# Performance work log

Hardware: AMD Instinct MI355X
Metric: run time of the kernel (lower is better)

## Reference

```python
import jax, jax.numpy as jnp
import numpy as np

NUM_PROTEINS = 19000
NUM_DRUGS = 4000
NUM_CELL_LINES = 16
BATCH = 4096
NUM_EDGES = 40000
LAYERS = [2048, 1024, 1]
IN_DIM = 2 * (NUM_PROTEINS + NUM_CELL_LINES)  # 38032


def setup_inputs() -> dict:
    key = jax.random.key(0)
    ks = jax.random.split(key, 10)
    inp = {
        "drug_pairs": jax.random.randint(ks[0], (BATCH, 2), 0, NUM_DRUGS, dtype=jnp.int64 if jax.config.jax_enable_x64 else jnp.int32),
        "cell_lines": jax.random.randint(ks[1], (BATCH,), 0, NUM_CELL_LINES),
        "dpi_drug": jax.random.randint(ks[2], (NUM_EDGES,), 0, NUM_DRUGS),
        "dpi_prot": jax.random.randint(ks[3], (NUM_EDGES,), 0, NUM_PROTEINS),
        "W0": jax.random.normal(ks[4], (LAYERS[0], IN_DIM), dtype=jnp.float32) * 0.02,
        "b0": jnp.zeros((LAYERS[0],), dtype=jnp.float32),
        "W1": jax.random.normal(ks[5], (LAYERS[1], LAYERS[0]), dtype=jnp.float32) * 0.02,
        "b1": jnp.zeros((LAYERS[1],), dtype=jnp.float32),
        "W2": jax.random.normal(ks[6], (LAYERS[2], LAYERS[1]), dtype=jnp.float32) * 0.02,
        "b2": jnp.zeros((LAYERS[2],), dtype=jnp.float32),
    }
    return inp


def _mlp(x, W0, b0, W1, b1, W2, b2):
    h = jax.nn.relu(x @ W0.T + b0)
    h = jax.nn.relu(h @ W1.T + b1)
    return h @ W2.T + b2


def reference(drug_pairs, cell_lines, dpi_drug, dpi_prot, W0, b0, W1, b1, W2, b2):
    # Build drug -> protein multi-hot table with a single vectorized scatter
    # (replaces the per-row Python loop: prot[i, targets] = 1)
    table = jnp.zeros((NUM_DRUGS, NUM_PROTEINS), dtype=jnp.float32)
    table = table.at[dpi_drug, dpi_prot].set(1.0)

    prot_1 = table[drug_pairs[:, 0]]  # [B, P]
    prot_2 = table[drug_pairs[:, 1]]  # [B, P]
    one_hot_cl = jax.nn.one_hot(cell_lines, NUM_CELL_LINES, dtype=jnp.float32)  # [B, C]

    bd1 = jnp.concatenate([prot_1, one_hot_cl], axis=1)
    bd2 = jnp.concatenate([prot_2, one_hot_cl], axis=1)
    x1 = jnp.concatenate([bd1, bd2], axis=1)  # [B, 2*(P+C)]
    x2 = jnp.concatenate([bd2, bd1], axis=1)

    out1 = _mlp(x1, W0, b0, W1, b1, W2, b2)
    out2 = _mlp(x2, W0, b0, W1, b1, W2, b2)
    return (out1[:, 0], out2[:, 0])
```

## Files before the change

### kernel.cpp

```cpp
#include <hip/hip_runtime.h>
#include <hip/hip_bf16.h>
#include <stdint.h>

#define NPROT 19000
#define NDRUG 4000
#define NCELL 16
#define BATCH 4096
#define NEDGE 40000
#define L0 2048
#define L1DIM 1024
#define INDIM 38032
#define HALFDIM 19016
#define DCAP 96
#define BMWORDS ((NDRUG * NPROT + 31) / 32)
#define PSPLIT 9504
#define WSLOT 9504
#define WSTN2 9512

typedef float f32x4 __attribute__((ext_vector_type(4)));
typedef short s16x8 __attribute__((ext_vector_type(8)));

__global__ void zero_all_kernel(int* __restrict__ p, int n) {
    int i = blockIdx.x * 256 + threadIdx.x;
    if (i < n) p[i] = 0;
}

__global__ void scatter_dedup_kernel(const int* __restrict__ drug, const int* __restrict__ prot,
                                     unsigned* __restrict__ bitmap, int* __restrict__ cnt2,
                                     int* __restrict__ cntTot, unsigned short* __restrict__ dlist) {
    int e = blockIdx.x * 256 + threadIdx.x;
    if (e < NEDGE) {
        int d = drug[e], p = prot[e];
        unsigned idx = (unsigned)d * NPROT + p;
        unsigned bit = 1u << (idx & 31u);
        unsigned old = atomicOr(&bitmap[idx >> 5], bit);
        if (!(old & bit)) {
            int ph = p >= PSPLIT;
            atomicAdd(&cnt2[d * 2 + ph], 1);
            int pos = atomicAdd(&cntTot[d], 1);
            if (pos < DCAP) dlist[d * DCAP + pos] = (unsigned short)p;
        }
    }
}

__global__ __launch_bounds__(512) void stream_meta_kernel(const int* __restrict__ cnt2,
                                                          int* __restrict__ wlen,
                                                          int* __restrict__ wbase,
                                                          int* __restrict__ pref,
                                                          int* __restrict__ tcnt) {
    __shared__ int wl[16];
    int t = threadIdx.x;
    if (t < 16) wl[t] = 0;
    __syncthreads();
    int c0 = 0, c1 = 0;
#pragma unroll
    for (int k = 0; k < 8; ++k) {
        int d = t + (k << 9);
        pref[((t << 3) + k) * 2 + 0] = c0;
        pref[((t << 3) + k) * 2 + 1] = c1;
        if (d < NDRUG) {
            int n0 = cnt2[d * 2], n1 = cnt2[d * 2 + 1];
            c0 += n0 ? n0 : 1;
            c1 += n1 ? n1 : 1;
        }
    }
    tcnt[t * 2] = c0;
    tcnt[t * 2 + 1] = c1;
    atomicMax(&wl[(t >> 6) * 2], c0);
    atomicMax(&wl[(t >> 6) * 2 + 1], c1);
    __syncthreads();
    if (t == 0) {
        int run = 0;
        for (int s = 0; s < 16; ++s) {
            wlen[s] = wl[s];
            wbase[s] = run;
            run += wl[s] * 64;
        }
    }
}

__global__ __launch_bounds__(256) void fill_stream_kernel(const int* __restrict__ cnt2,
                                                          const unsigned short* __restrict__ dlist,
                                                          const int* __restrict__ wbase,
                                                          const int* __restrict__ wlen,
                                                          const int* __restrict__ pref,
                                                          const int* __restrict__ tcnt,
                                                          unsigned short* __restrict__ estream) {
    int g = blockIdx.x * 256 + threadIdx.x;
    if (g < NDRUG) {
        int d = g;
        int t = d & 511, k = d >> 9;
        int wv = t >> 6, lane = t & 63;
        int n0 = cnt2[d * 2], n1 = cnt2[d * 2 + 1];
        int base0 = wbase[wv * 2 + 0] + lane;
        int base1 = wbase[wv * 2 + 1] + lane;
        int i0 = pref[((t << 3) + k) * 2 + 0];
        int i1 = pref[((t << 3) + k) * 2 + 1];
        int n = min(n0 + n1, DCAP);
        int j0 = 0, j1 = 0;
        for (int i = 0; i < n; ++i) {
            int p = dlist[d * DCAP + i];
            if (p < PSPLIT) {
                unsigned short e = (unsigned short)(p | ((j0 == n0 - 1) ? 0x8000 : 0));
                estream[base0 + (i0 + j0) * 64] = e;
                ++j0;
            } else {
                unsigned short e = (unsigned short)((p - PSPLIT) | ((j1 == n1 - 1) ? 0x8000 : 0));
                estream[base1 + (i1 + j1) * 64] = e;
                ++j1;
            }
        }
        if (n0 == 0) estream[base0 + i0 * 64] = (unsigned short)(WSLOT | 0x8000);
        if (n1 == 0) estream[base1 + i1 * 64] = (unsigned short)(WSLOT | 0x8000);
    } else if (g < NDRUG + 1024) {
        int idx = g - NDRUG;
        int t = idx >> 1, ph = idx & 1;
        int wv = t >> 6;
        int base = wbase[wv * 2 + ph] + (t & 63);
        int wl = wlen[wv * 2 + ph];
        for (int j = tcnt[t * 2 + ph]; j < wl; ++j)
            estream[base + j * 64] = (unsigned short)WSLOT;
    }
}

__global__ void base_kernel(const float* __restrict__ W0, const float* __restrict__ b0,
                            float* __restrict__ BASE) {
    int i = blockIdx.x * 256 + threadIdx.x;
    if (i < NCELL * L0) {
        int c = i >> 11, ch = i & 2047;
        const float* wr = W0 + (size_t)ch * INDIM;
        BASE[(size_t)c * L0 + ch] = b0[ch] + wr[NPROT + c] + wr[HALFDIM + NPROT + c];
    }
}

__device__ inline unsigned bfpair(float a, float b) {
    unsigned ua = __float_as_uint(a), ub = __float_as_uint(b);
    ua += 0x7fffu + ((ua >> 16) & 1u);
    ub += 0x7fffu + ((ub >> 16) & 1u);
    return (ua >> 16) | (ub & 0xffff0000u);
}
__device__ inline float bflo(unsigned w) { return __uint_as_float(w << 16); }
__device__ inline float bfhi(unsigned w) { return __uint_as_float(w & 0xffff0000u); }

__global__ __launch_bounds__(512) void drug_sum_kernel(const float* __restrict__ W0,
                                                       const unsigned short* __restrict__ estream,
                                                       const int* __restrict__ wbase,
                                                       const int* __restrict__ wlen,
                                                       uint2* __restrict__ SAT) {
    __shared__ uint2 wst[WSTN2];
    int t = threadIdx.x;
    int bid = blockIdx.x;
    int ph = bid >> 10;
    int k3 = bid & 1023;
    int hb = k3 >> 9;
    int quad = k3 & 511;
    int ch0 = quad * 4;
    size_t colbase = (size_t)hb * HALFDIM + (size_t)ph * PSPLIT;
    int pc = ph ? (NPROT - PSPLIT) : PSPLIT;

    int wv = t >> 6;
    int sid = wv * 2 + ph;
    int base = wbase[sid] + (t & 63);
    int wl = wlen[sid];
    int nfull = wl >> 3, rem = wl & 7;
    unsigned e[8];
    if (nfull > 0) {
#pragma unroll
        for (int k = 0; k < 8; ++k) e[k] = estream[base + k * 64];
        base += 512;
    }

    const float* sA = W0 + (size_t)(ch0 + 0) * INDIM + colbase;
    const float* sB = W0 + (size_t)(ch0 + 1) * INDIM + colbase;
    const float* sC = W0 + (size_t)(ch0 + 2) * INDIM + colbase;
    const float* sD = W0 + (size_t)(ch0 + 3) * INDIM + colbase;
#pragma unroll
    for (int k = 0; k < 4; ++k) {
        int i = t * 4 + k * 2048;
        float4 a = *(const float4*)(sA + i);
        float4 b = *(const float4*)(sB + i);
        float4 c = *(const float4*)(sC + i);
        float4 d = *(const float4*)(sD + i);
        uint4 q0, q1;
        q0.x = bfpair(a.x, b.x); q0.y = bfpair(c.x, d.x);
        q0.z = bfpair(a.y, b.y); q0.w = bfpair(c.y, d.y);
        q1.x = bfpair(a.z, b.z); q1.y = bfpair(c.z, d.z);
        q1.z = bfpair(a.w, b.w); q1.w = bfpair(c.w, d.w);
        *(uint4*)&wst[i] = q0;
        *(uint4*)&wst[i + 2] = q1;
    }
    {
        int i = t * 4 + 8192;
        if (i < pc) {
            float4 a = *(const float4*)(sA + i);
            float4 b = *(const float4*)(sB + i);
            float4 c = *(const float4*)(sC + i);
            float4 d = *(const float4*)(sD + i);
            uint4 q0, q1;
            q0.x = bfpair(a.x, b.x); q0.y = bfpair(c.x, d.x);
            q0.z = bfpair(a.y, b.y); q0.w = bfpair(c.y, d.y);
            q1.x = bfpair(a.z, b.z); q1.y = bfpair(c.z, d.z);
            q1.z = bfpair(a.w, b.w); q1.w = bfpair(c.w, d.w);
            *(uint4*)&wst[i] = q0;
            *(uint4*)&wst[i + 2] = q1;
        }
    }
    if (t < 8) { wst[WSLOT + t].x = 0u; wst[WSLOT + t].y = 0u; }
    __syncthreads();

    float x0 = 0.f, x1 = 0.f, x2 = 0.f, x3 = 0.f;
    int kk = 0;
    uint2* dstT = SAT + (size_t)bid * 4096;

    auto procBatch = [&](const unsigned* ev) {
        uint2 w[8];
#pragma unroll
        for (int k = 0; k < 8; ++k) w[k] = wst[ev[k] & 0x7fffu];
#pragma unroll
        for (int k = 0; k < 8; ++k) {
            x0 += bflo(w[k].x);
            x1 += bfhi(w[k].x);
            x2 += bflo(w[k].y);
            x3 += bfhi(w[k].y);
            if (ev[k] & 0x8000u) {
                uint2 v;
                v.x = bfpair(x0, x1);
                v.y = bfpair(x2, x3);
                dstT[t + (kk << 9)] = v;
                ++kk; x0 = 0.f; x1 = 0.f; x2 = 0.f; x3 = 0.f;
            }
        }
    };

    if (nfull > 0) {
        for (int it = 1; it < nfull; ++it) {
            unsigned f[8];
#pragma unroll
            for (int k = 0; k < 8; ++k) f[k] = estream[base + k * 64];
            base += 512;
            procBatch(e);
#pragma unroll
            for (int k = 0; k < 8; ++k) e[k] = f[k];
        }
        procBatch(e);
    }
    for (int k = 0; k < rem; ++k) {
        unsigned ev = estream[base + k * 64];
        uint2 w = wst[ev & 0x7fffu];
        x0 += bflo(w.x);
        x1 += bfhi(w.x);
        x2 += bflo(w.y);
        x3 += bfhi(w.y);
        if (ev & 0x8000u) {
            uint2 v;
            v.x = bfpair(x0, x1);
            v.y = bfpair(x2, x3);
            dstT[t + (kk << 9)] = v;
            ++kk; x0 = 0.f; x1 = 0.f; x2 = 0.f; x3 = 0.f;
        }
    }
}

__global__ __launch_bounds__(256) void combine_kernel(const uint2* __restrict__ SAT,
                                                      __hip_bfloat16* __restrict__ SAb,
                                                      __hip_bfloat16* __restrict__ SBb) {
    __shared__ float tile[4][32][33];
    int b = blockIdx.x;
    int hb = b / 2000;
    int rem = b % 2000;
    int q0 = (rem / 125) * 32;
    int d0 = (rem % 125) * 32;
    const uint2* inA = SAT + (size_t)(hb * 512) * 4096;
    const uint2* inB = SAT + (size_t)(1024 + hb * 512) * 4096;
    int tx = threadIdx.x & 31, ty = threadIdx.x >> 5;
#pragma unroll
    for (int r = 0; r < 32; r += 8) {
        int q = q0 + r + ty;
        uint2 a = inA[(size_t)q * 4096 + d0 + tx];
        uint2 c = inB[(size_t)q * 4096 + d0 + tx];
        tile[0][r + ty][tx] = bflo(a.x) + bflo(c.x);
        tile[1][r + ty][tx] = bfhi(a.x) + bfhi(c.x);
        tile[2][r + ty][tx] = bflo(a.y) + bflo(c.y);
        tile[3][r + ty][tx] = bfhi(a.y) + bfhi(c.y);
    }
    __syncthreads();
    __hip_bfloat16* out = hb ? SBb : SAb;
#pragma unroll
    for (int r = 0; r < 32; r += 8) {
        int d = d0 + r + ty;
        float x = tile[0][tx][r + ty];
        float y = tile[1][tx][r + ty];
        float z = tile[2][tx][r + ty];
        float w = tile[3][tx][r + ty];
        uint2 v;
        v.x = bfpair(x, y);
        v.y = bfpair(z, w);
        *(uint2*)(out + (size_t)d * L0 + (q0 + tx) * 4) = v;
    }
}

__global__ void cvtw1_kernel(const float* __restrict__ W1, __hip_bfloat16* __restrict__ W1b) {
    int i = blockIdx.x * 256 + threadIdx.x;
    const int n = L1DIM * L0 / 4;
    if (i < n) {
        float4 v = ((const float4*)W1)[i];
        uint2 q;
        q.x = bfpair(v.x, v.y);
        q.y = bfpair(v.z, v.w);
        ((uint2*)W1b)[i] = q;
    }
}

__global__ __launch_bounds__(256) void build_h_kernel(const int* __restrict__ dp,
                                                      const int* __restrict__ cl,
                                                      const __hip_bfloat16* __restrict__ SAb,
                                                      const __hip_bfloat16* __restrict__ SBb,
                                                      const float* __restrict__ BASE,
                                                      __hip_bfloat16* __restrict__ h1) {
    int b = blockIdx.x;
    int d1 = dp[2 * b], d2 = dp[2 * b + 1], c = cl[b];
    int ch = threadIdx.x * 8;
    const float* bs = BASE + (size_t)c * L0 + ch;
    uint4 ua1 = *(const uint4*)(SAb + (size_t)d1 * L0 + ch);
    uint4 ua2 = *(const uint4*)(SAb + (size_t)d2 * L0 + ch);
    uint4 us1 = *(const uint4*)(SBb + (size_t)d1 * L0 + ch);
    uint4 us2 = *(const uint4*)(SBb + (size_t)d2 * L0 + ch);
    float4 vb0 = *(const float4*)(bs);
    float4 vb1 = *(const float4*)(bs + 4);
    float bsv[8] = {vb0.x, vb0.y, vb0.z, vb0.w, vb1.x, vb1.y, vb1.z, vb1.w};
    unsigned a1w[4] = {ua1.x, ua1.y, ua1.z, ua1.w};
    unsigned a2w[4] = {ua2.x, ua2.y, ua2.z, ua2.w};
    unsigned s1w[4] = {us1.x, us1.y, us1.z, us1.w};
    unsigned s2w[4] = {us2.x, us2.y, us2.z, us2.w};
    float z1[8], z2[8];
#pragma unroll
    for (int k = 0; k < 4; ++k) {
        z1[2 * k]     = fmaxf(bsv[2 * k]     + bflo(a1w[k]) + bflo(s2w[k]), 0.f);
        z1[2 * k + 1] = fmaxf(bsv[2 * k + 1] + bfhi(a1w[k]) + bfhi(s2w[k]), 0.f);
        z2[2 * k]     = fmaxf(bsv[2 * k]     + bflo(a2w[k]) + bflo(s1w[k]), 0.f);
        z2[2 * k + 1] = fmaxf(bsv[2 * k + 1] + bfhi(a2w[k]) + bfhi(s1w[k]), 0.f);
    }
    uint4 o1, o2;
    o1.x = bfpair(z1[0], z1[1]); o1.y = bfpair(z1[2], z1[3]);
    o1.z = bfpair(z1[4], z1[5]); o1.w = bfpair(z1[6], z1[7]);
    o2.x = bfpair(z2[0], z2[1]); o2.y = bfpair(z2[2], z2[3]);
    o2.z = bfpair(z2[4], z2[5]); o2.w = bfpair(z2[6], z2[7]);
    *(uint4*)((__hip_bfloat16*)h1 + (size_t)b * L0 + ch) = o1;
    *(uint4*)((__hip_bfloat16*)h1 + (size_t)(BATCH + b) * L0 + ch) = o2;
}

__global__ void init_out_kernel(float* __restrict__ out, const float* __restrict__ b2, int n) {
    int i = blockIdx.x * 256 + threadIdx.x;
    if (i < n) out[i] = b2[0];
}

#define BM 128
#define BN 128
#define BK2 64
__global__ __launch_bounds__(256) void gemm_kernel(const __hip_bfloat16* __restrict__ A,
                                                   const __hip_bfloat16* __restrict__ B,
                                                   const float* __restrict__ bias,
                                                   const float* __restrict__ W2,
                                                   float* __restrict__ out,
                                                   int M, int N, int K) {
    __shared__ __hip_bfloat16 As[BM * BK2];
    __shared__ __hip_bfloat16 Bs[BN * BK2];
    int t = threadIdx.x;
    int bid = blockIdx.x;
    int xcd = bid & 7, ii2 = bid >> 3;
    int by = xcd * 8 + (ii2 >> 3);
    int bx = ii2 & 7;
    int brow = by * BM, bcol = bx * BN;
    int w = t >> 6, l = t & 63;
    int wr = w >> 1, wc = w & 1;
    f32x4 acc[4][4] = {};
    int row = l & 15, ko = (l >> 4) * 8;
    int swz = (row & 7) * 8;
    for (int k0 = 0; k0 < K; k0 += BK2) {
#pragma unroll
        for (int i = 0; i < 4; ++i) {
            int idx = i * 256 + t;
            int r = idx >> 3;
            int cb = ((idx & 7) ^ (r & 7)) * 8;
            __builtin_amdgcn_global_load_lds(
                (const __attribute__((address_space(1))) void*)(A + (size_t)(brow + r) * K + k0 + cb),
                (__attribute__((address_space(3))) void*)(&As[idx * 8]), 16, 0, 0);
            __builtin_amdgcn_global_load_lds(
                (const __attribute__((address_space(1))) void*)(B + (size_t)(bcol + r) * K + k0 + cb),
                (__attribute__((address_space(3))) void*)(&Bs[idx * 8]), 16, 0, 0);
        }
        __syncthreads();
#pragma unroll
        for (int ks = 0; ks < 2; ++ks) {
            int col = (ks * 32 + ko) ^ swz;
            s16x8 af[4], bfr[4];
#pragma unroll
            for (int m = 0; m < 4; ++m)
                af[m] = *(const s16x8*)(&As[(wr * 64 + m * 16 + row) * BK2 + col]);
#pragma unroll
            for (int n = 0; n < 4; ++n)
                bfr[n] = *(const s16x8*)(&Bs[(wc * 64 + n * 16 + row) * BK2 + col]);
#pragma unroll
            for (int m = 0; m < 4; ++m)
#pragma unroll
                for (int n = 0; n < 4; ++n)
                    acc[m][n] = __builtin_amdgcn_mfma_f32_16x16x32_bf16(af[m], bfr[n], acc[m][n], 0, 0, 0);
        }
        __syncthreads();
    }
    int cr = (l >> 4) * 4;
    int cc = l & 15;
#pragma unroll
    for (int m = 0; m < 4; ++m) {
        float s[4] = {0.f, 0.f, 0.f, 0.f};
#pragma unroll
        for (int n = 0; n < 4; ++n) {
            int gcol = bcol + wc * 64 + n * 16 + cc;
            float bv = bias[gcol];
            float wv = W2[gcol];
#pragma unroll
            for (int j = 0; j < 4; ++j) {
                float v = fmaxf(acc[m][n][j] + bv, 0.f);
                s[j] += v * wv;
            }
        }
#pragma unroll
        for (int mask = 1; mask < 16; mask <<= 1) {
#pragma unroll
            for (int j = 0; j < 4; ++j) s[j] += __shfl_xor(s[j], mask);
        }
        if (cc == 0) {
            int grow = brow + wr * 64 + m * 16 + cr;
#pragma unroll
            for (int j = 0; j < 4; ++j) atomicAdd(&out[grow + j], s[j]);
        }
    }
}

extern "C" void kernel_launch(void* const* d_in, const int* in_sizes, int n_in,
                              void* d_out, int out_size, void* d_ws, size_t ws_size,
                              hipStream_t stream) {
    const int* drug_pairs = (const int*)d_in[0];
    const int* cell_lines = (const int*)d_in[1];
    const int* dpi_drug = (const int*)d_in[2];
    const int* dpi_prot = (const int*)d_in[3];
    const float* W0 = (const float*)d_in[4];
    const float* b0 = (const float*)d_in[5];
    const float* W1 = (const float*)d_in[6];
    const float* b1 = (const float*)d_in[7];
    const float* W2 = (const float*)d_in[8];
    const float* b2 = (const float*)d_in[9];
    float* out = (float*)d_out;

    char* ws = (char*)d_ws;
    size_t off = 0;
    auto alloc = [&](size_t bytes) {
        char* p = ws + off;
        off += (bytes + 255) & ~(size_t)255;
        return p;
    };
    __hip_bfloat16* SAb = (__hip_bfloat16*)alloc((size_t)NDRUG * L0 * 2);
    __hip_bfloat16* SBb = (__hip_bfloat16*)alloc((size_t)NDRUG * L0 * 2);
    uint2* SAT = (uint2*)alloc((size_t)2048 * 4096 * 8);
    float* BASE = (float*)alloc((size_t)NCELL * L0 * 4);
    __hip_bfloat16* W1b = (__hip_bfloat16*)alloc((size_t)L1DIM * L0 * 2);
    __hip_bfloat16* h1 = (__hip_bfloat16*)alloc((size_t)2 * BATCH * L0 * 2);
    const int ZREG_N = BMWORDS + 3 * NDRUG;
    int* zreg = (int*)alloc((size_t)ZREG_N * 4);
    unsigned* bitmap = (unsigned*)zreg;
    int* cnt2 = zreg + BMWORDS;
    int* cntTot = zreg + BMWORDS + 2 * NDRUG;
    unsigned short* dlist = (unsigned short*)alloc((size_t)NDRUG * DCAP * 2);
    int* wlen = (int*)alloc(16 * 4);
    int* wbase = (int*)alloc(16 * 4);
    int* pref = (int*)alloc((size_t)512 * 8 * 2 * 4);
    int* tcnt = (int*)alloc((size_t)512 * 2 * 4);
    unsigned short* estream = (unsigned short*)alloc((size_t)64 * (NEDGE + 2 * NDRUG + 2048) * 2);

    zero_all_kernel<<<(ZREG_N + 255) / 256, 256, 0, stream>>>(zreg, ZREG_N);
    scatter_dedup_kernel<<<(NEDGE + 255) / 256, 256, 0, stream>>>(dpi_drug, dpi_prot,
                                                                  bitmap, cnt2, cntTot, dlist);
    stream_meta_kernel<<<1, 512, 0, stream>>>(cnt2, wlen, wbase, pref, tcnt);
    fill_stream_kernel<<<(NDRUG + 1024 + 255) / 256, 256, 0, stream>>>(cnt2, dlist, wbase,
                                                                       wlen, pref, tcnt, estream);
    base_kernel<<<(NCELL * L0 + 255) / 256, 256, 0, stream>>>(W0, b0, BASE);
    drug_sum_kernel<<<2048, 512, 0, stream>>>(W0, estream, wbase, wlen, SAT);
    combine_kernel<<<4000, 256, 0, stream>>>(SAT, SAb, SBb);
    cvtw1_kernel<<<(L1DIM * L0 / 4 + 255) / 256, 256, 0, stream>>>(W1, W1b);
    build_h_kernel<<<BATCH, 256, 0, stream>>>(drug_pairs, cell_lines, SAb, SBb, BASE, h1);
    init_out_kernel<<<(2 * BATCH + 255) / 256, 256, 0, stream>>>(out, b2, 2 * BATCH);
    gemm_kernel<<<(2 * BATCH / BM) * (L1DIM / BN), 256, 0, stream>>>(h1, W1b, b1, W2, out,
                                                                     2 * BATCH, L1DIM, L0);
}
```

Baseline: 216.7 us.

## Stage W0 channel pairs into LDS via direct global-to-LDS loads in fp32

The drug-sum kernel now handles two output channels per block instead of four. It copies the fp32 W0 rows straight into shared memory with global_load_lds, dropping the register round-trip and the bf16 packing during staging. Accumulation reads fp32 from LDS in two planes, and combine_kernel is adapted to the packed pair format. This doubles the block count and the SAT intermediate traffic in partial-sum launches, in exchange for cheaper staging and higher occupancy per block.

```diff
diff --git a/kernel.cpp b/kernel.cpp
--- a/kernel.cpp
+++ b/kernel.cpp
@@ -15,7 +15,7 @@
 #define BMWORDS ((NDRUG * NPROT + 31) / 32)
 #define PSPLIT 9504
 #define WSLOT 9504
-#define WSTN2 9512
+#define CPB 9512
 
 typedef float f32x4 __attribute__((ext_vector_type(4)));
 typedef short s16x8 __attribute__((ext_vector_type(8)));
@@ -146,17 +146,16 @@
                                                        const unsigned short* __restrict__ estream,
                                                        const int* __restrict__ wbase,
                                                        const int* __restrict__ wlen,
-                                                       uint2* __restrict__ SAT) {
-    __shared__ uint2 wst[WSTN2];
+                                                       unsigned* __restrict__ SAT) {
+    __shared__ float wst[2 * CPB];
     int t = threadIdx.x;
     int bid = blockIdx.x;
-    int ph = bid >> 10;
-    int k3 = bid & 1023;
-    int hb = k3 >> 9;
-    int quad = k3 & 511;
-    int ch0 = quad * 4;
+    int ph = bid >> 11;
+    int k3 = bid & 2047;
+    int hb = k3 >> 10;
+    int cp = k3 & 1023;
+    int ch0 = cp * 2;
     size_t colbase = (size_t)hb * HALFDIM + (size_t)ph * PSPLIT;
-    int pc = ph ? (NPROT - PSPLIT) : PSPLIT;
 
     int wv = t >> 6;
     int sid = wv * 2 + ph;
@@ -170,64 +169,38 @@
         base += 512;
     }
 
-    const float* sA = W0 + (size_t)(ch0 + 0) * INDIM + colbase;
-    const float* sB = W0 + (size_t)(ch0 + 1) * INDIM + colbase;
-    const float* sC = W0 + (size_t)(ch0 + 2) * INDIM + colbase;
-    const float* sD = W0 + (size_t)(ch0 + 3) * INDIM + colbase;
-#pragma unroll
-    for (int k = 0; k < 4; ++k) {
-        int i = t * 4 + k * 2048;
-        float4 a = *(const float4*)(sA + i);
-        float4 b = *(const float4*)(sB + i);
-        float4 c = *(const float4*)(sC + i);
-        float4 d = *(const float4*)(sD + i);
-        uint4 q0, q1;
-        q0.x = bfpair(a.x, b.x); q0.y = bfpair(c.x, d.x);
-        q0.z = bfpair(a.y, b.y); q0.w = bfpair(c.y, d.y);
-        q1.x = bfpair(a.z, b.z); q1.y = bfpair(c.z, d.z);
-        q1.z = bfpair(a.w, b.w); q1.w = bfpair(c.w, d.w);
-        *(uint4*)&wst[i] = q0;
-        *(uint4*)&wst[i + 2] = q1;
-    }
-    {
-        int i = t * 4 + 8192;
-        if (i < pc) {
-            float4 a = *(const float4*)(sA + i);
-            float4 b = *(const float4*)(sB + i);
-            float4 c = *(const float4*)(sC + i);
-            float4 d = *(const float4*)(sD + i);
-            uint4 q0, q1;
-            q0.x = bfpair(a.x, b.x); q0.y = bfpair(c.x, d.x);
-            q0.z = bfpair(a.y, b.y); q0.w = bfpair(c.y, d.y);
-            q1.x = bfpair(a.z, b.z); q1.y = bfpair(c.z, d.z);
-            q1.z = bfpair(a.w, b.w); q1.w = bfpair(c.w, d.w);
-            *(uint4*)&wst[i] = q0;
-            *(uint4*)&wst[i + 2] = q1;
-        }
-    }
-    if (t < 8) { wst[WSLOT + t].x = 0u; wst[WSLOT + t].y = 0u; }
+    const float* s0 = W0 + (size_t)ch0 * INDIM + colbase;
+    const float* s1 = W0 + (size_t)(ch0 + 1) * INDIM + colbase;
+    for (int i = t * 4; i < PSPLIT; i += 2048) {
+        __builtin_amdgcn_global_load_lds(
+            (const __attribute__((address_space(1))) void*)(s0 + i),
+            (__attribute__((address_space(3))) void*)(&wst[i]), 16, 0, 0);
+        __builtin_amdgcn_global_load_lds(
+            (const __attribute__((address_space(1))) void*)(s1 + i),
+            (__attribute__((address_space(3))) void*)(&wst[CPB + i]), 16, 0, 0);
+    }
+    if (t < 8) { wst[WSLOT + t] = 0.f; wst[CPB + WSLOT + t] = 0.f; }
     __syncthreads();
 
-    float x0 = 0.f, x1 = 0.f, x2 = 0.f, x3 = 0.f;
+    float x0 = 0.f, x1 = 0.f;
     int kk = 0;
-    uint2* dstT = SAT + (size_t)bid * 4096;
+    unsigned* dstT = SAT + (size_t)bid * 4096;
 
     auto procBatch = [&](const unsigned* ev) {
-        uint2 w[8];
-#pragma unroll
-        for (int k = 0; k < 8; ++k) w[k] = wst[ev[k] & 0x7fffu];
+        float w0[8], w1[8];
 #pragma unroll
         for (int k = 0; k < 8; ++k) {
-            x0 += bflo(w[k].x);
-            x1 += bfhi(w[k].x);
-            x2 += bflo(w[k].y);
-            x3 += bfhi(w[k].y);
+            int p = ev[k] & 0x7fffu;
+            w0[k] = wst[p];
+            w1[k] = wst[CPB + p];
+        }
+#pragma unroll
+        for (int k = 0; k < 8; ++k) {
+            x0 += w0[k];
+            x1 += w1[k];
             if (ev[k] & 0x8000u) {
-                uint2 v;
-                v.x = bfpair(x0, x1);
-                v.y = bfpair(x2, x3);
-                dstT[t + (kk << 9)] = v;
-                ++kk; x0 = 0.f; x1 = 0.f; x2 = 0.f; x3 = 0.f;
+                dstT[t + (kk << 9)] = bfpair(x0, x1);
+                ++kk; x0 = 0.f; x1 = 0.f;
             }
         }
     };
@@ -246,42 +219,33 @@
     }
     for (int k = 0; k < rem; ++k) {
         unsigned ev = estream[base + k * 64];
-        uint2 w = wst[ev & 0x7fffu];
-        x0 += bflo(w.x);
-        x1 += bfhi(w.x);
-        x2 += bflo(w.y);
-        x3 += bfhi(w.y);
+        int p = ev & 0x7fffu;
+        x0 += wst[p];
+        x1 += wst[CPB + p];
         if (ev & 0x8000u) {
-            uint2 v;
-            v.x = bfpair(x0, x1);
-            v.y = bfpair(x2, x3);
-            dstT[t + (kk << 9)] = v;
-            ++kk; x0 = 0.f; x1 = 0.f; x2 = 0.f; x3 = 0.f;
-        }
-    }
-}
-
-__global__ __launch_bounds__(256) void combine_kernel(const uint2* __restrict__ SAT,
+            dstT[t + (kk << 9)] = bfpair(x0, x1);
+            ++kk; x0 = 0.f; x1 = 0.f;
+        }
+    }
+}
+
+__global__ __launch_bounds__(256) void combine_kernel(const unsigned* __restrict__ SAT,
                                                       __hip_bfloat16* __restrict__ SAb,
                                                       __hip_bfloat16* __restrict__ SBb) {
-    __shared__ float tile[4][32][33];
+    __shared__ float tile[2][32][33];
     int b = blockIdx.x;
-    int hb = b / 2000;
-    int rem = b % 2000;
-    int q0 = (rem / 125) * 32;
+    int hb = b / 4000;
+    int rem = b % 4000;
+    int c0 = (rem / 125) * 32;
     int d0 = (rem % 125) * 32;
-    const uint2* inA = SAT + (size_t)(hb * 512) * 4096;
-    const uint2* inB = SAT + (size_t)(1024 + hb * 512) * 4096;
     int tx = threadIdx.x & 31, ty = threadIdx.x >> 5;
 #pragma unroll
     for (int r = 0; r < 32; r += 8) {
-        int q = q0 + r + ty;
-        uint2 a = inA[(size_t)q * 4096 + d0 + tx];
-        uint2 c = inB[(size_t)q * 4096 + d0 + tx];
-        tile[0][r + ty][tx] = bflo(a.x) + bflo(c.x);
-        tile[1][r + ty][tx] = bfhi(a.x) + bfhi(c.x);
-        tile[2][r + ty][tx] = bflo(a.y) + bflo(c.y);
-        tile[3][r + ty][tx] = bfhi(a.y) + bfhi(c.y);
+        int cp = c0 + r + ty;
+        unsigned a = SAT[(size_t)(hb * 1024 + cp) * 4096 + d0 + tx];
+        unsigned c = SAT[(size_t)(2048 + hb * 1024 + cp) * 4096 + d0 + tx];
+        tile[0][r + ty][tx] = bflo(a) + bflo(c);
+        tile[1][r + ty][tx] = bfhi(a) + bfhi(c);
     }
     __syncthreads();
     __hip_bfloat16* out = hb ? SBb : SAb;
@@ -290,12 +254,8 @@
         int d = d0 + r + ty;
         float x = tile[0][tx][r + ty];
         float y = tile[1][tx][r + ty];
-        float z = tile[2][tx][r + ty];
-        float w = tile[3][tx][r + ty];
-        uint2 v;
-        v.x = bfpair(x, y);
-        v.y = bfpair(z, w);
-        *(uint2*)(out + (size_t)d * L0 + (q0 + tx) * 4) = v;
+        unsigned v = bfpair(x, y);
+        *(unsigned*)(out + (size_t)d * L0 + (c0 + tx) * 2) = v;
     }
 }
 
@@ -461,7 +421,7 @@
     };
     __hip_bfloat16* SAb = (__hip_bfloat16*)alloc((size_t)NDRUG * L0 * 2);
     __hip_bfloat16* SBb = (__hip_bfloat16*)alloc((size_t)NDRUG * L0 * 2);
-    uint2* SAT = (uint2*)alloc((size_t)2048 * 4096 * 8);
+    unsigned* SAT = (unsigned*)alloc((size_t)4096 * 4096 * 4);
     float* BASE = (float*)alloc((size_t)NCELL * L0 * 4);
     __hip_bfloat16* W1b = (__hip_bfloat16*)alloc((size_t)L1DIM * L0 * 2);
     __hip_bfloat16* h1 = (__hip_bfloat16*)alloc((size_t)2 * BATCH * L0 * 2);
@@ -484,8 +444,8 @@
     fill_stream_kernel<<<(NDRUG + 1024 + 255) / 256, 256, 0, stream>>>(cnt2, dlist, wbase,
                                                                        wlen, pref, tcnt, estream);
     base_kernel<<<(NCELL * L0 + 255) / 256, 256, 0, stream>>>(W0, b0, BASE);
-    drug_sum_kernel<<<2048, 512, 0, stream>>>(W0, estream, wbase, wlen, SAT);
-    combine_kernel<<<4000, 256, 0, stream>>>(SAT, SAb, SBb);
+    drug_sum_kernel<<<4096, 512, 0, stream>>>(W0, estream, wbase, wlen, SAT);
+    combine_kernel<<<8000, 256, 0, stream>>>(SAT, SAb, SBb);
     cvtw1_kernel<<<(L1DIM * L0 / 4 + 255) / 256, 256, 0, stream>>>(W1, W1b);
     build_h_kernel<<<BATCH, 256, 0, stream>>>(drug_pairs, cell_lines, SAb, SBb, BASE, h1);
     init_out_kernel<<<(2 * BATCH + 255) / 256, 256, 0, stream>>>(out, b2, 2 * BATCH);
```

After: 222.8 us. 2.8% more time.

## Split protein range into four quarters with fp32 LDS staged via direct global-to-LDS loads

Applied to the files above, without the earlier changes.

Splits the protein dimension into four quarters instead of two, so each drug_sum block stages a smaller slice of W0. The slice stays in fp32 in LDS, one plane per output channel, loaded with global_load_lds instead of being converted to packed bf16 through registers. The smaller LDS footprint should allow more blocks per CU and removes the conversion work. In exchange the grid doubles, the SAT intermediate doubles in size, and combine_kernel must read and reduce four partial sums per element instead of two.

```diff
diff --git a/kernel.cpp b/kernel.cpp
--- a/kernel.cpp
+++ b/kernel.cpp
@@ -13,9 +13,9 @@
 #define HALFDIM 19016
 #define DCAP 96
 #define BMWORDS ((NDRUG * NPROT + 31) / 32)
-#define PSPLIT 9504
-#define WSLOT 9504
-#define WSTN2 9512
+#define PQ 4752
+#define QSLOT 4752
+#define QSTRIDE 4760
 
 typedef float f32x4 __attribute__((ext_vector_type(4)));
 typedef short s16x8 __attribute__((ext_vector_type(8)));
@@ -26,7 +26,7 @@
 }
 
 __global__ void scatter_dedup_kernel(const int* __restrict__ drug, const int* __restrict__ prot,
-                                     unsigned* __restrict__ bitmap, int* __restrict__ cnt2,
+                                     unsigned* __restrict__ bitmap, int* __restrict__ cnt4,
                                      int* __restrict__ cntTot, unsigned short* __restrict__ dlist) {
     int e = blockIdx.x * 256 + threadIdx.x;
     if (e < NEDGE) {
@@ -35,43 +35,53 @@
         unsigned bit = 1u << (idx & 31u);
         unsigned old = atomicOr(&bitmap[idx >> 5], bit);
         if (!(old & bit)) {
-            int ph = p >= PSPLIT;
-            atomicAdd(&cnt2[d * 2 + ph], 1);
+            int q = p / PQ;
+            atomicAdd(&cnt4[d * 4 + q], 1);
             int pos = atomicAdd(&cntTot[d], 1);
             if (pos < DCAP) dlist[d * DCAP + pos] = (unsigned short)p;
         }
     }
 }
 
-__global__ __launch_bounds__(512) void stream_meta_kernel(const int* __restrict__ cnt2,
+__global__ __launch_bounds__(512) void stream_meta_kernel(const int* __restrict__ cnt4,
                                                           int* __restrict__ wlen,
                                                           int* __restrict__ wbase,
                                                           int* __restrict__ pref,
                                                           int* __restrict__ tcnt) {
-    __shared__ int wl[16];
+    __shared__ int wl[32];
     int t = threadIdx.x;
-    if (t < 16) wl[t] = 0;
+    if (t < 32) wl[t] = 0;
     __syncthreads();
-    int c0 = 0, c1 = 0;
+    int c0 = 0, c1 = 0, c2 = 0, c3 = 0;
 #pragma unroll
     for (int k = 0; k < 8; ++k) {
         int d = t + (k << 9);
-        pref[((t << 3) + k) * 2 + 0] = c0;
-        pref[((t << 3) + k) * 2 + 1] = c1;
+        int pb = ((t << 3) + k) * 4;
+        pref[pb + 0] = c0;
+        pref[pb + 1] = c1;
+        pref[pb + 2] = c2;
+        pref[pb + 3] = c3;
         if (d < NDRUG) {
-            int n0 = cnt2[d * 2], n1 = cnt2[d * 2 + 1];
+            int n0 = cnt4[d * 4 + 0], n1 = cnt4[d * 4 + 1];
+            int n2 = cnt4[d * 4 + 2], n3 = cnt4[d * 4 + 3];
             c0 += n0 ? n0 : 1;
             c1 += n1 ? n1 : 1;
-        }
-    }
-    tcnt[t * 2] = c0;
-    tcnt[t * 2 + 1] = c1;
-    atomicMax(&wl[(t >> 6) * 2], c0);
-    atomicMax(&wl[(t >> 6) * 2 + 1], c1);
+            c2 += n2 ? n2 : 1;
+            c3 += n3 ? n3 : 1;
+        }
+    }
+    tcnt[t * 4 + 0] = c0;
+    tcnt[t * 4 + 1] = c1;
+    tcnt[t * 4 + 2] = c2;
+    tcnt[t * 4 + 3] = c3;
+    atomicMax(&wl[(t >> 6) * 4 + 0], c0);
+    atomicMax(&wl[(t >> 6) * 4 + 1], c1);
+    atomicMax(&wl[(t >> 6) * 4 + 2], c2);
+    atomicMax(&wl[(t >> 6) * 4 + 3], c3);
     __syncthreads();
     if (t == 0) {
         int run = 0;
-        for (int s = 0; s < 16; ++s) {
+        for (int s = 0; s < 32; ++s) {
             wlen[s] = wl[s];
             wbase[s] = run;
             run += wl[s] * 64;
@@ -79,7 +89,7 @@
     }
 }
 
-__global__ __launch_bounds__(256) void fill_stream_kernel(const int* __restrict__ cnt2,
+__global__ __launch_bounds__(256) void fill_stream_kernel(const int* __restrict__ cnt4,
                                                           const unsigned short* __restrict__ dlist,
                                                           const int* __restrict__ wbase,
                                                           const int* __restrict__ wlen,
@@ -91,35 +101,34 @@
         int d = g;
         int t = d & 511, k = d >> 9;
         int wv = t >> 6, lane = t & 63;
-        int n0 = cnt2[d * 2], n1 = cnt2[d * 2 + 1];
-        int base0 = wbase[wv * 2 + 0] + lane;
-        int base1 = wbase[wv * 2 + 1] + lane;
-        int i0 = pref[((t << 3) + k) * 2 + 0];
-        int i1 = pref[((t << 3) + k) * 2 + 1];
-        int n = min(n0 + n1, DCAP);
-        int j0 = 0, j1 = 0;
-        for (int i = 0; i < n; ++i) {
+        int n[4], bases[4], idx[4], j[4];
+#pragma unroll
+        for (int q = 0; q < 4; ++q) {
+            n[q] = cnt4[d * 4 + q];
+            bases[q] = wbase[wv * 4 + q] + lane;
+            idx[q] = pref[((t << 3) + k) * 4 + q];
+            j[q] = 0;
+        }
+        int ntot = min(n[0] + n[1] + n[2] + n[3], DCAP);
+        for (int i = 0; i < ntot; ++i) {
             int p = dlist[d * DCAP + i];
-            if (p < PSPLIT) {
-                unsigned short e = (unsigned short)(p | ((j0 == n0 - 1) ? 0x8000 : 0));
-                estream[base0 + (i0 + j0) * 64] = e;
-                ++j0;
-            } else {
-                unsigned short e = (unsigned short)((p - PSPLIT) | ((j1 == n1 - 1) ? 0x8000 : 0));
-                estream[base1 + (i1 + j1) * 64] = e;
-                ++j1;
-            }
-        }
-        if (n0 == 0) estream[base0 + i0 * 64] = (unsigned short)(WSLOT | 0x8000);
-        if (n1 == 0) estream[base1 + i1 * 64] = (unsigned short)(WSLOT | 0x8000);
-    } else if (g < NDRUG + 1024) {
+            int q = p / PQ;
+            int lp = p - q * PQ;
+            unsigned short e = (unsigned short)(lp | ((j[q] == n[q] - 1) ? 0x8000 : 0));
+            estream[bases[q] + (idx[q] + j[q]) * 64] = e;
+            j[q]++;
+        }
+#pragma unroll
+        for (int q = 0; q < 4; ++q)
+            if (n[q] == 0) estream[bases[q] + idx[q] * 64] = (unsigned short)(QSLOT | 0x8000);
+    } else if (g < NDRUG + 2048) {
         int idx = g - NDRUG;
-        int t = idx >> 1, ph = idx & 1;
+        int t = idx >> 2, q = idx & 3;
         int wv = t >> 6;
-        int base = wbase[wv * 2 + ph] + (t & 63);
-        int wl = wlen[wv * 2 + ph];
-        for (int j = tcnt[t * 2 + ph]; j < wl; ++j)
-            estream[base + j * 64] = (unsigned short)WSLOT;
+        int base = wbase[wv * 4 + q] + (t & 63);
+        int wlq = wlen[wv * 4 + q];
+        for (int jj = tcnt[t * 4 + q]; jj < wlq; ++jj)
+            estream[base + jj * 64] = (unsigned short)QSLOT;
     }
 }
 
@@ -147,19 +156,18 @@
                                                        const int* __restrict__ wbase,
                                                        const int* __restrict__ wlen,
                                                        uint2* __restrict__ SAT) {
-    __shared__ uint2 wst[WSTN2];
+    __shared__ float wst[4 * QSTRIDE];
     int t = threadIdx.x;
     int bid = blockIdx.x;
-    int ph = bid >> 10;
+    int pq = bid >> 10;
     int k3 = bid & 1023;
     int hb = k3 >> 9;
     int quad = k3 & 511;
     int ch0 = quad * 4;
-    size_t colbase = (size_t)hb * HALFDIM + (size_t)ph * PSPLIT;
-    int pc = ph ? (NPROT - PSPLIT) : PSPLIT;
+    size_t colbase = (size_t)hb * HALFDIM + (size_t)pq * PQ;
 
     int wv = t >> 6;
-    int sid = wv * 2 + ph;
+    int sid = wv * 4 + pq;
     int base = wbase[sid] + (t & 63);
     int wl = wlen[sid];
     int nfull = wl >> 3, rem = wl & 7;
@@ -170,42 +178,16 @@
         base += 512;
     }
 
-    const float* sA = W0 + (size_t)(ch0 + 0) * INDIM + colbase;
-    const float* sB = W0 + (size_t)(ch0 + 1) * INDIM + colbase;
-    const float* sC = W0 + (size_t)(ch0 + 2) * INDIM + colbase;
-    const float* sD = W0 + (size_t)(ch0 + 3) * INDIM + colbase;
-#pragma unroll
-    for (int k = 0; k < 4; ++k) {
-        int i = t * 4 + k * 2048;
-        float4 a = *(const float4*)(sA + i);
-        float4 b = *(const float4*)(sB + i);
-        float4 c = *(const float4*)(sC + i);
-        float4 d = *(const float4*)(sD + i);
-        uint4 q0, q1;
-        q0.x = bfpair(a.x, b.x); q0.y = bfpair(c.x, d.x);
-        q0.z = bfpair(a.y, b.y); q0.w = bfpair(c.y, d.y);
-        q1.x = bfpair(a.z, b.z); q1.y = bfpair(c.z, d.z);
-        q1.z = bfpair(a.w, b.w); q1.w = bfpair(c.w, d.w);
-        *(uint4*)&wst[i] = q0;
-        *(uint4*)&wst[i + 2] = q1;
-    }
-    {
-        int i = t * 4 + 8192;
-        if (i < pc) {
-            float4 a = *(const float4*)(sA + i);
-            float4 b = *(const float4*)(sB + i);
-            float4 c = *(const float4*)(sC + i);
-            float4 d = *(const float4*)(sD + i);
-            uint4 q0, q1;
-            q0.x = bfpair(a.x, b.x); q0.y = bfpair(c.x, d.x);
-            q0.z = bfpair(a.y, b.y); q0.w = bfpair(c.y, d.y);
-            q1.x = bfpair(a.z, b.z); q1.y = bfpair(c.z, d.z);
-            q1.z = bfpair(a.w, b.w); q1.w = bfpair(c.w, d.w);
-            *(uint4*)&wst[i] = q0;
-            *(uint4*)&wst[i + 2] = q1;
-        }
-    }
-    if (t < 8) { wst[WSLOT + t].x = 0u; wst[WSLOT + t].y = 0u; }
+#pragma unroll
+    for (int c = 0; c < 4; ++c) {
+        const float* src = W0 + (size_t)(ch0 + c) * INDIM + colbase;
+        for (int i = t * 4; i < PQ; i += 2048) {
+            __builtin_amdgcn_global_load_lds(
+                (const __attribute__((address_space(1))) void*)(src + i),
+                (__attribute__((address_space(3))) void*)(&wst[c * QSTRIDE + i]), 16, 0, 0);
+        }
+    }
+    if (t < 32) wst[(t >> 3) * QSTRIDE + QSLOT + (t & 7)] = 0.f;
     __syncthreads();
 
     float x0 = 0.f, x1 = 0.f, x2 = 0.f, x3 = 0.f;
@@ -213,15 +195,21 @@
     uint2* dstT = SAT + (size_t)bid * 4096;
 
     auto procBatch = [&](const unsigned* ev) {
-        uint2 w[8];
-#pragma unroll
-        for (int k = 0; k < 8; ++k) w[k] = wst[ev[k] & 0x7fffu];
+        float w0[8], w1[8], w2[8], w3[8];
 #pragma unroll
         for (int k = 0; k < 8; ++k) {
-            x0 += bflo(w[k].x);
-            x1 += bfhi(w[k].x);
-            x2 += bflo(w[k].y);
-            x3 += bfhi(w[k].y);
+            int p = ev[k] & 0x7fffu;
+            w0[k] = wst[p];
+            w1[k] = wst[QSTRIDE + p];
+            w2[k] = wst[2 * QSTRIDE + p];
+            w3[k] = wst[3 * QSTRIDE + p];
+        }
+#pragma unroll
+        for (int k = 0; k < 8; ++k) {
+            x0 += w0[k];
+            x1 += w1[k];
+            x2 += w2[k];
+            x3 += w3[k];
             if (ev[k] & 0x8000u) {
                 uint2 v;
                 v.x = bfpair(x0, x1);
@@ -246,11 +234,11 @@
     }
     for (int k = 0; k < rem; ++k) {
         unsigned ev = estream[base + k * 64];
-        uint2 w = wst[ev & 0x7fffu];
-        x0 += bflo(w.x);
-        x1 += bfhi(w.x);
-        x2 += bflo(w.y);
-        x3 += bfhi(w.y);
+        int p = ev & 0x7fffu;
+        x0 += wst[p];
+        x1 += wst[QSTRIDE + p];
+        x2 += wst[2 * QSTRIDE + p];
+        x3 += wst[3 * QSTRIDE + p];
         if (ev & 0x8000u) {
             uint2 v;
             v.x = bfpair(x0, x1);
@@ -270,18 +258,23 @@
     int rem = b % 2000;
     int q0 = (rem / 125) * 32;
     int d0 = (rem % 125) * 32;
-    const uint2* inA = SAT + (size_t)(hb * 512) * 4096;
-    const uint2* inB = SAT + (size_t)(1024 + hb * 512) * 4096;
     int tx = threadIdx.x & 31, ty = threadIdx.x >> 5;
 #pragma unroll
     for (int r = 0; r < 32; r += 8) {
-        int q = q0 + r + ty;
-        uint2 a = inA[(size_t)q * 4096 + d0 + tx];
-        uint2 c = inB[(size_t)q * 4096 + d0 + tx];
-        tile[0][r + ty][tx] = bflo(a.x) + bflo(c.x);
-        tile[1][r + ty][tx] = bfhi(a.x) + bfhi(c.x);
-        tile[2][r + ty][tx] = bflo(a.y) + bflo(c.y);
-        tile[3][r + ty][tx] = bfhi(a.y) + bfhi(c.y);
+        int quad = q0 + r + ty;
+        float s0 = 0.f, s1 = 0.f, s2 = 0.f, s3 = 0.f;
+#pragma unroll
+        for (int pq = 0; pq < 4; ++pq) {
+            uint2 a = SAT[(size_t)(pq * 1024 + hb * 512 + quad) * 4096 + d0 + tx];
+            s0 += bflo(a.x);
+            s1 += bfhi(a.x);
+            s2 += bflo(a.y);
+            s3 += bfhi(a.y);
+        }
+        tile[0][r + ty][tx] = s0;
+        tile[1][r + ty][tx] = s1;
+        tile[2][r + ty][tx] = s2;
+        tile[3][r + ty][tx] = s3;
     }
     __syncthreads();
     __hip_bfloat16* out = hb ? SBb : SAb;
@@ -461,30 +454,30 @@
     };
     __hip_bfloat16* SAb = (__hip_bfloat16*)alloc((size_t)NDRUG * L0 * 2);
     __hip_bfloat16* SBb = (__hip_bfloat16*)alloc((size_t)NDRUG * L0 * 2);
-    uint2* SAT = (uint2*)alloc((size_t)2048 * 4096 * 8);
+    uint2* SAT = (uint2*)alloc((size_t)4096 * 4096 * 8);
     float* BASE = (float*)alloc((size_t)NCELL * L0 * 4);
     __hip_bfloat16* W1b = (__hip_bfloat16*)alloc((size_t)L1DIM * L0 * 2);
     __hip_bfloat16* h1 = (__hip_bfloat16*)alloc((size_t)2 * BATCH * L0 * 2);
-    const int ZREG_N = BMWORDS + 3 * NDRUG;
+    const int ZREG_N = BMWORDS + 5 * NDRUG;
     int* zreg = (int*)alloc((size_t)ZREG_N * 4);
     unsigned* bitmap = (unsigned*)zreg;
-    int* cnt2 = zreg + BMWORDS;
-    int* cntTot = zreg + BMWORDS + 2 * NDRUG;
+    int* cnt4 = zreg + BMWORDS;
+    int* cntTot = zreg + BMWORDS + 4 * NDRUG;
     unsigned short* dlist = (unsigned short*)alloc((size_t)NDRUG * DCAP * 2);
-    int* wlen = (int*)alloc(16 * 4);
-    int* wbase = (int*)alloc(16 * 4);
-    int* pref = (int*)alloc((size_t)512 * 8 * 2 * 4);
-    int* tcnt = (int*)alloc((size_t)512 * 2 * 4);
-    unsigned short* estream = (unsigned short*)alloc((size_t)64 * (NEDGE + 2 * NDRUG + 2048) * 2);
+    int* wlen = (int*)alloc(32 * 4);
+    int* wbase = (int*)alloc(32 * 4);
+    int* pref = (int*)alloc((size_t)512 * 8 * 4 * 4);
+    int* tcnt = (int*)alloc((size_t)512 * 4 * 4);
+    unsigned short* estream = (unsigned short*)alloc((size_t)64 * (NEDGE + 4 * NDRUG + 4096) * 2);
 
     zero_all_kernel<<<(ZREG_N + 255) / 256, 256, 0, stream>>>(zreg, ZREG_N);
     scatter_dedup_kernel<<<(NEDGE + 255) / 256, 256, 0, stream>>>(dpi_drug, dpi_prot,
-                                                                  bitmap, cnt2, cntTot, dlist);
-    stream_meta_kernel<<<1, 512, 0, stream>>>(cnt2, wlen, wbase, pref, tcnt);
-    fill_stream_kernel<<<(NDRUG + 1024 + 255) / 256, 256, 0, stream>>>(cnt2, dlist, wbase,
+                                                                  bitmap, cnt4, cntTot, dlist);
+    stream_meta_kernel<<<1, 512, 0, stream>>>(cnt4, wlen, wbase, pref, tcnt);
+    fill_stream_kernel<<<(NDRUG + 2048 + 255) / 256, 256, 0, stream>>>(cnt4, dlist, wbase,
                                                                        wlen, pref, tcnt, estream);
     base_kernel<<<(NCELL * L0 + 255) / 256, 256, 0, stream>>>(W0, b0, BASE);
-    drug_sum_kernel<<<2048, 512, 0, stream>>>(W0, estream, wbase, wlen, SAT);
+    drug_sum_kernel<<<4096, 512, 0, stream>>>(W0, estream, wbase, wlen, SAT);
     combine_kernel<<<4000, 256, 0, stream>>>(SAT, SAb, SBb);
     cvtw1_kernel<<<(L1DIM * L0 / 4 + 255) / 256, 256, 0, stream>>>(W1, W1b);
     build_h_kernel<<<BATCH, 256, 0, stream>>>(drug_pairs, cell_lines, SAb, SBb, BASE, h1);
```

Result: slower. 242.6 us (+12.0%).
